# Optimization experiments

Hardware: AMD Instinct MI355X
Metric: run time of the kernel (lower is better)

## Reference

```python
import jax, jax.numpy as jnp
import numpy as np

B, L, D, A, OUT, HID_FC = 4, 4096, 128, 16, 2, 24


def setup_inputs() -> dict:
    key = jax.random.key(0)
    ks = jax.random.split(key, 8)
    xn = lambda k, shape: (jax.random.normal(k, shape, dtype=jnp.float32)
                           * np.sqrt(2.0 / (shape[0] + shape[1])))
    return {
        "x": jax.random.normal(ks[0], (B, L, D), dtype=jnp.float32),
        "fc1_w": xn(ks[1], (D, D)),
        "fc1_b": jnp.zeros((D,), dtype=jnp.float32),
        "Wq_w": xn(ks[2], (D, D)),
        "Wk_w": xn(ks[3], (D, D)),
        "Wv_w": xn(ks[4], (D, D)),
        "fc2_w": xn(ks[5], (D, HID_FC)),
        "fc2_b": jnp.zeros((HID_FC,), dtype=jnp.float32),
        "fc3_w": xn(ks[6], (HID_FC, OUT)),
        "fc3_b": jnp.zeros((OUT,), dtype=jnp.float32),
        "atten_size": A,
        "hidden_size": D,
    }


def _attention(x, Wq_w, Wk_w, Wv_w, atten_size, sqrt_hidden):
    b, l, d = x.shape
    W = 2 * atten_size + 1
    # zero-pad sequence dim, then gather local windows.
    # Faithful to roll-based construction: x_nei[b,i,j] = x[b, i + atten_size - j] (0 if out of range)
    padded = jnp.pad(x, ((0, 0), (atten_size, atten_size), (0, 0)))
    idx = jnp.arange(l)[:, None] + 2 * atten_size - jnp.arange(W)[None, :]  # [L, W]
    x_nei = padded[:, idx]                      # [B, L, W, D]
    q = (x @ Wq_w)[:, :, None, :]               # [B, L, 1, D]
    k = x_nei @ Wk_w                            # [B, L, W, D]
    dsc = jnp.einsum('blod,blwd->blow', q, k) / sqrt_hidden  # [B, L, 1, W]
    # Original torch code: Softmax(dim=2) over the singleton dim -> all-ones (faithful)
    a = jax.nn.softmax(dsc, axis=2)             # [B, L, 1, W]
    v = x_nei @ Wv_w                            # [B, L, W, D]
    out = jnp.squeeze(a @ v, axis=2)            # [B, L, D]
    return out, a


def reference(x, fc1_w, fc1_b, Wq_w, Wk_w, Wv_w, fc2_w, fc2_b, fc3_w, fc3_b,
              atten_size, hidden_size):
    sqrt_hidden = np.sqrt(float(hidden_size))
    h = jax.nn.relu(x @ fc1_w + fc1_b)
    h, a = _attention(h, Wq_w, Wk_w, Wv_w, atten_size, sqrt_hidden)
    h = jax.nn.relu(h @ fc2_w + fc2_b)
    out = h @ fc3_w + fc3_b
    return out, a
```

## Files before the change

kernel.cpp:

```cpp
#include <hip/hip_runtime.h>

constexpr int Bv   = 4;
constexpr int Lv   = 4096;
constexpr int Dv   = 128;
constexpr int Av   = 16;
constexpr int Wwin = 2*Av + 1;
constexpr int OUTv = 2;
constexpr int HIDv = 24;
constexpr int NROWS = Bv * Lv;

constexpr int TILE  = 32;
constexpr int SROWS = TILE + 2*Av;
constexpr int NBLK  = NROWS / TILE;

typedef __attribute__((ext_vector_type(8))) short short8;
typedef __attribute__((ext_vector_type(4))) short short4v;
typedef __attribute__((ext_vector_type(4))) float f32x4;

__device__ __forceinline__ short f2bf(float f) {
    unsigned u = __builtin_bit_cast(unsigned, f);
    u += 0x7FFFu + ((u >> 16) & 1u);
    return (short)(u >> 16);
}

__global__ __launch_bounds__(256) void k_all(const float* __restrict__ x,
                                             const float* __restrict__ W1,
                                             const float* __restrict__ b1,
                                             const float* __restrict__ Wv,
                                             const float* __restrict__ fc2,
                                             const float* __restrict__ fc2b,
                                             const float* __restrict__ fc3w,
                                             const float* __restrict__ fc3b,
                                             float* __restrict__ out,
                                             float* __restrict__ aout) {
    __shared__ short sA[SROWS][136];
    __shared__ short sWfT[32][136];
    __shared__ float smv[SROWS][25];
    __shared__ float sh2[TILE][25];
    __shared__ float sb1[Dv];

    const int t = threadIdx.x, blk = blockIdx.x;
    const int g0 = blk * TILE;
    const int bb = g0 >> 12;
    const int l0 = g0 & (Lv - 1);
    const int lane = t & 63, w = t >> 6;
    const int arow = lane & 15;
    const int kgrp = (lane >> 4) * 8;
    const int crow = (lane >> 4) * 4;

    for (int i = t; i < SROWS*32; i += 256) {
        const int r = i >> 5, c4 = i & 31;
        const int l = l0 - Av + r;
        short4v o = {0, 0, 0, 0};
        if (l >= 0 && l < Lv) {
            const float4 v = *(const float4*)&x[((size_t)bb*Lv + l)*Dv + c4*4];
            o[0] = f2bf(v.x); o[1] = f2bf(v.y); o[2] = f2bf(v.z); o[3] = f2bf(v.w);
        }
        *(short4v*)&sA[r][c4*4] = o;
    }
    if (t < Dv) sb1[t] = b1[t];

    {
        float4* a4 = (float4*)aout;
        const float4 one4 = {1.f, 1.f, 1.f, 1.f};
        for (int i = t; i < 264; i += 256)
            a4[(size_t)blk*264 + i] = one4;
    }

    {
        f32x4 accW[2][2];
#pragma unroll
        for (int a = 0; a < 2; ++a) { accW[a][0] = (f32x4){0,0,0,0}; accW[a][1] = (f32x4){0,0,0,0}; }
#pragma unroll
        for (int kb = 0; kb < 4; ++kb) {
            const int kof = kb*32 + kgrp;
            short8 bW[2];
#pragma unroll
            for (int nf = 0; nf < 2; ++nf) {
                const int n = nf*16 + arow;
#pragma unroll
                for (int j = 0; j < 8; ++j) {
                    const float v = (n < HIDv) ? fc2[(size_t)(kof + j)*HIDv + n] : 0.f;
                    bW[nf][j] = f2bf(v);
                }
            }
#pragma unroll
            for (int mf2 = 0; mf2 < 2; ++mf2) {
                const int m = (w*2 + mf2)*16 + arow;
                const float4 v0 = *(const float4*)&Wv[(size_t)m*Dv + kof];
                const float4 v1 = *(const float4*)&Wv[(size_t)m*Dv + kof + 4];
                short8 aW;
                aW[0] = f2bf(v0.x); aW[1] = f2bf(v0.y); aW[2] = f2bf(v0.z); aW[3] = f2bf(v0.w);
                aW[4] = f2bf(v1.x); aW[5] = f2bf(v1.y); aW[6] = f2bf(v1.z); aW[7] = f2bf(v1.w);
                accW[mf2][0] = __builtin_amdgcn_mfma_f32_16x16x32_bf16(aW, bW[0], accW[mf2][0], 0, 0, 0);
                accW[mf2][1] = __builtin_amdgcn_mfma_f32_16x16x32_bf16(aW, bW[1], accW[mf2][1], 0, 0, 0);
            }
        }
#pragma unroll
        for (int mf2 = 0; mf2 < 2; ++mf2) {
#pragma unroll
            for (int nf = 0; nf < 2; ++nf) {
                const int n = nf*16 + arow;
                const int m = (w*2 + mf2)*16 + crow;
                short4v o;
                o[0] = f2bf(accW[mf2][nf][0]);
                o[1] = f2bf(accW[mf2][nf][1]);
                o[2] = f2bf(accW[mf2][nf][2]);
                o[3] = f2bf(accW[mf2][nf][3]);
                *(short4v*)&sWfT[n][m] = o;
            }
        }
    }
    __syncthreads();

    const int ncol0 = w * 32;
    f32x4 acc[4][2];
#pragma unroll
    for (int mf = 0; mf < 4; ++mf) { acc[mf][0] = (f32x4){0,0,0,0}; acc[mf][1] = (f32x4){0,0,0,0}; }

#pragma unroll
    for (int kb = 0; kb < 4; ++kb) {
        const int kof = kb*32 + kgrp;
        short8 bf0, bf1;
        {
            const int n0 = ncol0 + arow, n1 = ncol0 + 16 + arow;
#pragma unroll
            for (int j = 0; j < 8; ++j) {
                bf0[j] = f2bf(W1[(size_t)(kof + j)*Dv + n0]);
                bf1[j] = f2bf(W1[(size_t)(kof + j)*Dv + n1]);
            }
        }
#pragma unroll
        for (int mf = 0; mf < 4; ++mf) {
            const short8 af = *(const short8*)&sA[mf*16 + arow][kof];
            acc[mf][0] = __builtin_amdgcn_mfma_f32_16x16x32_bf16(af, bf0, acc[mf][0], 0, 0, 0);
            acc[mf][1] = __builtin_amdgcn_mfma_f32_16x16x32_bf16(af, bf1, acc[mf][1], 0, 0, 0);
        }
    }
    __syncthreads();

#pragma unroll
    for (int mf = 0; mf < 4; ++mf) {
#pragma unroll
        for (int nf = 0; nf < 2; ++nf) {
            const int col  = ncol0 + nf*16 + arow;
            const float bias = sb1[col];
#pragma unroll
            for (int r = 0; r < 4; ++r) {
                float h = acc[mf][nf][r] + bias;
                h = h > 0.f ? h : 0.f;
                sA[mf*16 + crow + r][col] = f2bf(h);
            }
        }
    }
    __syncthreads();

    f32x4 acc2[2];
    acc2[0] = (f32x4){0,0,0,0};
    acc2[1] = (f32x4){0,0,0,0};
#pragma unroll
    for (int pp = 0; pp < 2; ++pp) {
        const int p = w*2 + pp, mf = p >> 1, nf = p & 1;
#pragma unroll
        for (int kb = 0; kb < 4; ++kb) {
            const int kof = kb*32 + kgrp;
            const short8 af = *(const short8*)&sA[mf*16 + arow][kof];
            const short8 bf = *(const short8*)&sWfT[nf*16 + arow][kof];
            acc2[pp] = __builtin_amdgcn_mfma_f32_16x16x32_bf16(af, bf, acc2[pp], 0, 0, 0);
        }
    }
#pragma unroll
    for (int pp = 0; pp < 2; ++pp) {
        const int p = w*2 + pp, mf = p >> 1, nf = p & 1;
        const int col = nf*16 + arow;
        if (col < HIDv) {
#pragma unroll
            for (int r = 0; r < 4; ++r) {
                const int row = mf*16 + crow + r;
                const int l = l0 - Av + row;
                smv[row][col] = (l >= 0 && l < Lv) ? acc2[pp][r] : 0.f;
            }
        }
    }
    __syncthreads();

    if (t < 96) {
        const int c = t % 24, rg = t / 24;
        const int rb = rg * 8;
        float s = 0.f;
#pragma unroll
        for (int ww = 0; ww < Wwin; ++ww) s += smv[rb + ww][c];
        const float bias = fc2b[c];
#pragma unroll
        for (int r2 = 0; r2 < 8; ++r2) {
            const int rr = rb + r2;
            const float h = s + bias;
            sh2[rr][c] = h > 0.f ? h : 0.f;
            if (r2 < 7) s += smv[rr + Wwin][c] - smv[rr][c];
        }
    }
    __syncthreads();

    if (t < TILE*OUTv) {
        const int r = t >> 1, oc = t & 1;
        float a = fc3b[oc];
#pragma unroll
        for (int c = 0; c < HIDv; ++c)
            a = fmaf(sh2[r][c], fc3w[c*OUTv + oc], a);
        out[(size_t)(g0 + r)*OUTv + oc] = a;
    }
}

extern "C" void kernel_launch(void* const* d_in, const int* in_sizes, int n_in,
                              void* d_out, int out_size, void* d_ws, size_t ws_size,
                              hipStream_t stream) {
    const float* x     = (const float*)d_in[0];
    const float* fc1_w = (const float*)d_in[1];
    const float* fc1_b = (const float*)d_in[2];
    const float* Wv_w  = (const float*)d_in[5];
    const float* fc2_w = (const float*)d_in[6];
    const float* fc2_b = (const float*)d_in[7];
    const float* fc3_w = (const float*)d_in[8];
    const float* fc3_b = (const float*)d_in[9];

    float* out  = (float*)d_out;
    float* aout = (float*)d_out + NROWS * OUTv;

    k_all<<<dim3(NBLK), dim3(256), 0, stream>>>(x, fc1_w, fc1_b, Wv_w, fc2_w,
                                                fc2_b, fc3_w, fc3_b, out, aout);
}
```

Baseline: 16.39 us.

## Use packed bf16 conversion intrinsics and remap block IDs per XCD

Replaces the hand-written scalar float-to-bf16 rounding with the HIP __float22bfloat162_rn packed conversion, so pairs of values can be converted with fewer ALU ops on hardware that has a packed convert instruction. It also remaps blockIdx so each of the 8 XCDs processes a contiguous range of tiles, which should improve L2 locality for the overlapping halo rows. The remap assumes NBLK is divisible by 8, and the conversion gain depends on the compiler emitting the native instruction.

```diff
diff --git a/kernel.cpp b/kernel.cpp
--- a/kernel.cpp
+++ b/kernel.cpp
@@ -1,4 +1,5 @@
 #include <hip/hip_runtime.h>
+#include <hip/hip_bf16.h>
 
 constexpr int Bv   = 4;
 constexpr int Lv   = 4096;
@@ -12,15 +13,21 @@
 constexpr int TILE  = 32;
 constexpr int SROWS = TILE + 2*Av;
 constexpr int NBLK  = NROWS / TILE;
+constexpr int NXCD  = 8;
 
 typedef __attribute__((ext_vector_type(8))) short short8;
-typedef __attribute__((ext_vector_type(4))) short short4v;
+typedef __attribute__((ext_vector_type(4))) unsigned uint4v;
 typedef __attribute__((ext_vector_type(4))) float f32x4;
 
-__device__ __forceinline__ short f2bf(float f) {
-    unsigned u = __builtin_bit_cast(unsigned, f);
-    u += 0x7FFFu + ((u >> 16) & 1u);
-    return (short)(u >> 16);
+__device__ __forceinline__ unsigned pk2(float lo, float hi) {
+    union { __hip_bfloat162 h; unsigned u; } cvt;
+    cvt.h = __float22bfloat162_rn(make_float2(lo, hi));
+    return cvt.u;
+}
+__device__ __forceinline__ short bf1(float f) {
+    union { __hip_bfloat16 h; short s; } cvt;
+    cvt.h = __float2bfloat16(f);
+    return cvt.s;
 }
 
 __global__ __launch_bounds__(256) void k_all(const float* __restrict__ x,
@@ -39,7 +46,10 @@
     __shared__ float sh2[TILE][25];
     __shared__ float sb1[Dv];
 
-    const int t = threadIdx.x, blk = blockIdx.x;
+    const int t = threadIdx.x;
+    const int bid = blockIdx.x;
+    const int blk = (bid & (NXCD-1)) * (NBLK/NXCD) + (bid >> 3);
+
     const int g0 = blk * TILE;
     const int bb = g0 >> 12;
     const int l0 = g0 & (Lv - 1);
@@ -51,12 +61,13 @@
     for (int i = t; i < SROWS*32; i += 256) {
         const int r = i >> 5, c4 = i & 31;
         const int l = l0 - Av + r;
-        short4v o = {0, 0, 0, 0};
+        uint2 o = make_uint2(0u, 0u);
         if (l >= 0 && l < Lv) {
             const float4 v = *(const float4*)&x[((size_t)bb*Lv + l)*Dv + c4*4];
-            o[0] = f2bf(v.x); o[1] = f2bf(v.y); o[2] = f2bf(v.z); o[3] = f2bf(v.w);
-        }
-        *(short4v*)&sA[r][c4*4] = o;
+            o.x = pk2(v.x, v.y);
+            o.y = pk2(v.z, v.w);
+        }
+        *(uint2*)&sA[r][c4*4] = o;
     }
     if (t < Dv) sb1[t] = b1[t];
 
@@ -78,20 +89,20 @@
 #pragma unroll
             for (int nf = 0; nf < 2; ++nf) {
                 const int n = nf*16 + arow;
-#pragma unroll
-                for (int j = 0; j < 8; ++j) {
-                    const float v = (n < HIDv) ? fc2[(size_t)(kof + j)*HIDv + n] : 0.f;
-                    bW[nf][j] = f2bf(v);
-                }
+                float f[8];
+#pragma unroll
+                for (int j = 0; j < 8; ++j)
+                    f[j] = (n < HIDv) ? fc2[(size_t)(kof + j)*HIDv + n] : 0.f;
+                uint4v u = {pk2(f[0],f[1]), pk2(f[2],f[3]), pk2(f[4],f[5]), pk2(f[6],f[7])};
+                bW[nf] = __builtin_bit_cast(short8, u);
             }
 #pragma unroll
             for (int mf2 = 0; mf2 < 2; ++mf2) {
                 const int m = (w*2 + mf2)*16 + arow;
                 const float4 v0 = *(const float4*)&Wv[(size_t)m*Dv + kof];
                 const float4 v1 = *(const float4*)&Wv[(size_t)m*Dv + kof + 4];
-                short8 aW;
-                aW[0] = f2bf(v0.x); aW[1] = f2bf(v0.y); aW[2] = f2bf(v0.z); aW[3] = f2bf(v0.w);
-                aW[4] = f2bf(v1.x); aW[5] = f2bf(v1.y); aW[6] = f2bf(v1.z); aW[7] = f2bf(v1.w);
+                uint4v u = {pk2(v0.x,v0.y), pk2(v0.z,v0.w), pk2(v1.x,v1.y), pk2(v1.z,v1.w)};
+                const short8 aW = __builtin_bit_cast(short8, u);
                 accW[mf2][0] = __builtin_amdgcn_mfma_f32_16x16x32_bf16(aW, bW[0], accW[mf2][0], 0, 0, 0);
                 accW[mf2][1] = __builtin_amdgcn_mfma_f32_16x16x32_bf16(aW, bW[1], accW[mf2][1], 0, 0, 0);
             }
@@ -102,12 +113,10 @@
             for (int nf = 0; nf < 2; ++nf) {
                 const int n = nf*16 + arow;
                 const int m = (w*2 + mf2)*16 + crow;
-                short4v o;
-                o[0] = f2bf(accW[mf2][nf][0]);
-                o[1] = f2bf(accW[mf2][nf][1]);
-                o[2] = f2bf(accW[mf2][nf][2]);
-                o[3] = f2bf(accW[mf2][nf][3]);
-                *(short4v*)&sWfT[n][m] = o;
+                uint2 o;
+                o.x = pk2(accW[mf2][nf][0], accW[mf2][nf][1]);
+                o.y = pk2(accW[mf2][nf][2], accW[mf2][nf][3]);
+                *(uint2*)&sWfT[n][m] = o;
             }
         }
     }
@@ -121,20 +130,25 @@
 #pragma unroll
     for (int kb = 0; kb < 4; ++kb) {
         const int kof = kb*32 + kgrp;
-        short8 bf0, bf1;
+        short8 bf0, bf1v;
         {
             const int n0 = ncol0 + arow, n1 = ncol0 + 16 + arow;
+            float a0[8], a1[8];
 #pragma unroll
             for (int j = 0; j < 8; ++j) {
-                bf0[j] = f2bf(W1[(size_t)(kof + j)*Dv + n0]);
-                bf1[j] = f2bf(W1[(size_t)(kof + j)*Dv + n1]);
-            }
+                a0[j] = W1[(size_t)(kof + j)*Dv + n0];
+                a1[j] = W1[(size_t)(kof + j)*Dv + n1];
+            }
+            uint4v u0 = {pk2(a0[0],a0[1]), pk2(a0[2],a0[3]), pk2(a0[4],a0[5]), pk2(a0[6],a0[7])};
+            uint4v u1 = {pk2(a1[0],a1[1]), pk2(a1[2],a1[3]), pk2(a1[4],a1[5]), pk2(a1[6],a1[7])};
+            bf0  = __builtin_bit_cast(short8, u0);
+            bf1v = __builtin_bit_cast(short8, u1);
         }
 #pragma unroll
         for (int mf = 0; mf < 4; ++mf) {
             const short8 af = *(const short8*)&sA[mf*16 + arow][kof];
-            acc[mf][0] = __builtin_amdgcn_mfma_f32_16x16x32_bf16(af, bf0, acc[mf][0], 0, 0, 0);
-            acc[mf][1] = __builtin_amdgcn_mfma_f32_16x16x32_bf16(af, bf1, acc[mf][1], 0, 0, 0);
+            acc[mf][0] = __builtin_amdgcn_mfma_f32_16x16x32_bf16(af, bf0,  acc[mf][0], 0, 0, 0);
+            acc[mf][1] = __builtin_amdgcn_mfma_f32_16x16x32_bf16(af, bf1v, acc[mf][1], 0, 0, 0);
         }
     }
     __syncthreads();
@@ -149,7 +163,7 @@
             for (int r = 0; r < 4; ++r) {
                 float h = acc[mf][nf][r] + bias;
                 h = h > 0.f ? h : 0.f;
-                sA[mf*16 + crow + r][col] = f2bf(h);
+                sA[mf*16 + crow + r][col] = bf1(h);
             }
         }
     }
```

After: 17.71 us. 8.1% more time.
